# Kernel tuning notes

Measured on AMD Instinct MI355X. Metric: run time of the kernel, lower is better.

Reference implementation:

```python
import jax, jax.numpy as jnp
import numpy as np


def setup_inputs() -> dict:
    key = jax.random.key(0)
    x = jax.random.normal(key, (4, 5, 256, 32, 32), dtype=jnp.float32)
    return {"x": x, "beta": 1}


def reference(x, beta):
    # x: [B, L, D, H, W] -> [B, L, H, W, D] -> [B, L, N, D], N = H*W
    B, L, D, H, W = x.shape
    xf = jnp.transpose(x, (0, 1, 3, 4, 2)).reshape(B, L, H * W, D)
    # scores: [B, L, N, N]
    scores = jnp.einsum('blnd,blmd->blnm', xf, xf)
    # exp(beta*s)/sum == softmax(beta*s) along last axis (numerically stable form)
    attention = jax.nn.softmax(beta * scores, axis=-1)
    # (x.unsqueeze(2) * attn.unsqueeze(4)).sum(3) == attn @ x
    return jnp.einsum('blnm,blmd->blnd', attention, xf)
```

## Files before the change

kernel.cpp:

```cpp
#include <hip/hip_runtime.h>


typedef __attribute__((ext_vector_type(8))) short bf16x8;
typedef __attribute__((ext_vector_type(4))) float f32x4;
typedef __attribute__((ext_vector_type(16))) float f32x16;

#define GLD16(gp, lp) __builtin_amdgcn_global_load_lds( \
    (const __attribute__((address_space(1))) unsigned int*)(const void*)(gp), \
    (__attribute__((address_space(3))) unsigned int*)(void*)(lp), 16, 0, 0)

#define LDS_BARRIER() __asm__ volatile("s_waitcnt lgkmcnt(0)\ns_barrier" ::: "memory")
#define MEMFENCE()    __asm__ volatile("" ::: "memory")
#define WAIT_KDMA()   do { __asm__ volatile("s_waitcnt vmcnt(8)" ::: "memory"); \
                           __builtin_amdgcn_sched_barrier(0); } while (0)

__device__ __forceinline__ unsigned int pack_bf16_rne(float a, float b) {
    unsigned int ua = __float_as_uint(a); ua += 0x7FFFu + ((ua >> 16) & 1u);
    unsigned int ub = __float_as_uint(b); ub += 0x7FFFu + ((ub >> 16) & 1u);
    return (ua >> 16) | (ub & 0xFFFF0000u);
}
__device__ __forceinline__ unsigned int pack2_trunc(float lo, float hi) {
    return __builtin_amdgcn_perm(__float_as_uint(hi), __float_as_uint(lo), 0x07060302u);
}

__global__ __launch_bounds__(256) void prep_kernel(const float* __restrict__ x,
                                                   unsigned short* __restrict__ XT,
                                                   unsigned short* __restrict__ XV) {
    __shared__ __align__(16) unsigned char smem[16384];
    int bid = blockIdx.x;
    int t = threadIdx.x;
    if (bid < 640) {
        uint4* T = (uint4*)smem;
        int slice = bid >> 5, w = bid & 31;
        int cc0 = (w & 3) * 32, d0 = (w >> 2) * 32;
        const float* xs = x + slice * 262144;
        int ccl = t & 31, dr = t >> 5;
        #pragma unroll
        for (int p = 0; p < 4; ++p) {
            int dl = p * 8 + dr;
            const float* src = xs + (d0 + dl) * 1024 + (cc0 + ccl) * 8;
            float4 a = *(const float4*)(src);
            float4 b = *(const float4*)(src + 4);
            uint4 o;
            o.x = pack_bf16_rne(a.x, a.y); o.y = pack_bf16_rne(a.z, a.w);
            o.z = pack_bf16_rne(b.x, b.y); o.w = pack_bf16_rne(b.z, b.w);
            T[ccl * 32 + (dl ^ ccl)] = o;
        }
        __syncthreads();
        unsigned short* xv = XV + slice * 262144;
        int dl2 = t & 31, cr = t >> 5;
        #pragma unroll
        for (int p = 0; p < 4; ++p) {
            int ccl2 = p * 8 + cr;
            uint4 o = T[ccl2 * 32 + (dl2 ^ ccl2)];
            *(uint4*)(xv + ((cc0 + ccl2) * 256 + d0 + dl2) * 8) = o;
        }
    } else {
        unsigned long long* TX = (unsigned long long*)smem;
        int b = bid - 640;
        int slice = b >> 5, w = b & 31;
        int d0 = (w & 1) * 128, n0 = (w >> 1) * 64;
        const float* xs = x + slice * 262144;
        int nq = t & 15, dqh = t >> 4;
        #pragma unroll
        for (int p = 0; p < 2; ++p) {
            int dq = p * 16 + dqh;
            const float* src = xs + (d0 + dq * 4) * 1024 + n0 + nq * 4;
            float4 r0 = *(const float4*)(src);
            float4 r1 = *(const float4*)(src + 1024);
            float4 r2 = *(const float4*)(src + 2048);
            float4 r3 = *(const float4*)(src + 3072);
            const float* f0 = (const float*)&r0; const float* f1 = (const float*)&r1;
            const float* f2 = (const float*)&r2; const float* f3 = (const float*)&r3;
            #pragma unroll
            for (int j = 0; j < 4; ++j) {
                int nl2 = nq * 4 + j;
                unsigned long long q = (unsigned long long)pack_bf16_rne(f0[j], f1[j])
                    | ((unsigned long long)pack_bf16_rne(f2[j], f3[j]) << 32);
                TX[nl2 * 32 + (dq ^ (nl2 & 31))] = q;
            }
        }
        __syncthreads();
        unsigned short* xt = XT + slice * 262144;
        int ch = t & 15, nr = t >> 4;
        #pragma unroll
        for (int p = 0; p < 4; ++p) {
            int nl2 = p * 16 + nr;
            unsigned long long qlo = TX[nl2 * 32 + ((ch * 2) ^ (nl2 & 31))];
            unsigned long long qhi = TX[nl2 * 32 + ((ch * 2 + 1) ^ (nl2 & 31))];
            uint4 o = make_uint4((unsigned int)qlo, (unsigned int)(qlo >> 32),
                                 (unsigned int)qhi, (unsigned int)(qhi >> 32));
            *(uint4*)(xt + (n0 + nl2) * 256 + ((((d0 >> 3) + ch) ^ (nl2 & 7)) * 8)) = o;
        }
    }
}

__global__ __launch_bounds__(256, 2) void attn_kernel(const unsigned short* __restrict__ XT,
                                                      const unsigned short* __restrict__ XV,
                                                      const int* __restrict__ beta,
                                                      float* __restrict__ out) {
    __shared__ __align__(16) unsigned short Kmd[64 * 256];
    __shared__ __align__(16) unsigned short Qlds[48 * 256];
    __shared__ __align__(16) unsigned short Pb[2][64 * 64];
    float* Lpart = (float*)&Pb[0][0];
    float* Ltot  = (float*)&Pb[0][2048];

    int bid = blockIdx.x;
    int t = ((bid & 7) * 40) + (bid >> 3);
    int slice = t >> 4, qh = t & 15;

    int tid = threadIdx.x;
    int lane = tid & 63, wv = tid >> 6;
    int nl = lane & 15, g = lane >> 4;
    int lo = lane & 31, hi = lane >> 5;

    const unsigned short* xt_s = XT + slice * 262144;
    const unsigned short* xv_s = XV + slice * 262144;
    float cscale = (float)(beta[0]) * 1.44269504089f;

    auto kdma = [&](int kt) {
        const unsigned short* gk = xt_s + kt * 16384;
        #pragma unroll
        for (int i = 0; i < 8; ++i) {
            int ch = wv * 8 + i;
            GLD16(gk + ch * 512 + lane * 8, &Kmd[ch * 512]);
        }
    };

    kdma(0);
    {
        const unsigned short* gq = xt_s + (qh * 64 + 16) * 256;
        #pragma unroll
        for (int i = 0; i < 6; ++i) {
            int ch = wv * 6 + i;
            GLD16(gq + ch * 512 + lane * 8, &Qlds[ch * 512]);
        }
    }
    MEMFENCE();

    bf16x8 qf[8];
    float mcol[4];
    {
        int n = qh * 64 + nl;
        const unsigned short* qrow = xt_s + n * 256;
        float dg = 0.f;
        #pragma unroll
        for (int ks = 0; ks < 8; ++ks) {
            qf[ks] = *(const bf16x8*)(qrow + (((ks * 4 + g) ^ (n & 7)) * 8));
            const unsigned int* qu = (const unsigned int*)&qf[ks];
            #pragma unroll
            for (int w = 0; w < 4; ++w) {
                float flo = __uint_as_float(qu[w] << 16);
                float fhi = __uint_as_float(qu[w] & 0xFFFF0000u);
                dg = fmaf(flo, flo, dg);
                dg = fmaf(fhi, fhi, dg);
            }
        }
        dg += __shfl_xor(dg, 16);
        dg += __shfl_xor(dg, 32);
        mcol[0] = dg * cscale;
    }

    const unsigned short* vb = xv_s + (hi * 256 + wv * 64 + lo) * 8;
    bf16x8 vf[8];
    MEMFENCE();
    #pragma unroll
    for (int ks = 0; ks < 4; ++ks) {
        vf[ks * 2]     = *(const bf16x8*)(vb + ks * 4096);
        vf[ks * 2 + 1] = *(const bf16x8*)(vb + ks * 4096 + 256);
    }
    __asm__ volatile("s_waitcnt vmcnt(8)" ::: "memory");
    __builtin_amdgcn_sched_barrier(0);
    LDS_BARRIER();

    #pragma unroll
    for (int st = 1; st < 4; ++st) {
        const unsigned short* qrow = &Qlds[((st - 1) * 16 + nl) * 256];
        float dg = 0.f;
        #pragma unroll
        for (int ks = 0; ks < 8; ++ks) {
            bf16x8 qv = *(const bf16x8*)(qrow + (((ks * 4 + g) ^ (nl & 7)) * 8));
            const unsigned int* qu = (const unsigned int*)&qv;
            #pragma unroll
            for (int w = 0; w < 4; ++w) {
                float flo = __uint_as_float(qu[w] << 16);
                float fhi = __uint_as_float(qu[w] & 0xFFFF0000u);
                dg = fmaf(flo, flo, dg);
                dg = fmaf(fhi, fhi, dg);
            }
        }
        dg += __shfl_xor(dg, 16);
        dg += __shfl_xor(dg, 32);
        mcol[st] = dg * cscale;
    }

    f32x16 acc[2][2];
    acc[0][0] = (f32x16)(0.f); acc[0][1] = (f32x16)(0.f);
    acc[1][0] = (f32x16)(0.f); acc[1][1] = (f32x16)(0.f);
    float lac[4] = {0.f, 0.f, 0.f, 0.f};

    const unsigned short* kmd_row = &Kmd[(wv * 16 + nl) * 256];
    const unsigned short* q1 = &Qlds[nl * 256];
    const unsigned short* q2 = &Qlds[(16 + nl) * 256];
    const unsigned short* q3 = &Qlds[(32 + nl) * 256];

    for (int kt = 0; kt < 16; ++kt) {
        WAIT_KDMA();

        f32x4 s0 = {0.f,0.f,0.f,0.f}, s1 = {0.f,0.f,0.f,0.f};
        f32x4 s2 = {0.f,0.f,0.f,0.f}, s3 = {0.f,0.f,0.f,0.f};
        #pragma unroll
        for (int ks = 0; ks < 8; ++ks) {
            int ch = ((ks * 4 + g) ^ (nl & 7)) * 8;
            bf16x8 af = *(const bf16x8*)(kmd_row + ch);
            s0 = __builtin_amdgcn_mfma_f32_16x16x32_bf16(af, qf[ks], s0, 0, 0, 0);
            s1 = __builtin_amdgcn_mfma_f32_16x16x32_bf16(af, *(const bf16x8*)(q1 + ch), s1, 0, 0, 0);
            s2 = __builtin_amdgcn_mfma_f32_16x16x32_bf16(af, *(const bf16x8*)(q2 + ch), s2, 0, 0, 0);
            s3 = __builtin_amdgcn_mfma_f32_16x16x32_bf16(af, *(const bf16x8*)(q3 + ch), s3, 0, 0, 0);
        }

        {
            f32x4 sv[4] = {s0, s1, s2, s3};
            #pragma unroll
            for (int st = 0; st < 4; ++st) {
                float p0 = exp2f(fmaf(sv[st][0], cscale, -mcol[st]));
                float p1 = exp2f(fmaf(sv[st][1], cscale, -mcol[st]));
                float p2 = exp2f(fmaf(sv[st][2], cscale, -mcol[st]));
                float p3 = exp2f(fmaf(sv[st][3], cscale, -mcol[st]));
                lac[st] += (p0 + p1) + (p2 + p3);
                *(uint2*)(&Pb[kt & 1][(st * 16 + nl) * 64 +
                                      (((wv * 2 + (g >> 1)) ^ (nl & 7)) * 8) + (g & 1) * 4]) =
                    make_uint2(pack2_trunc(p0, p1), pack2_trunc(p2, p3));
            }
        }

        if (kt < 15) kdma(kt + 1);
        MEMFENCE();

        LDS_BARRIER();

        {
            const unsigned short* vnext = vb + (kt + 1) * 16384;
            #pragma unroll
            for (int ks = 0; ks < 4; ++ks) {
                int ch = ((ks * 2 + hi) ^ (lo & 7)) * 8;
                bf16x8 pf0 = *(const bf16x8*)(&Pb[kt & 1][lo * 64 + ch]);
                bf16x8 pf1 = *(const bf16x8*)(&Pb[kt & 1][(32 + lo) * 64 + ch]);
                acc[0][0] = __builtin_amdgcn_mfma_f32_32x32x16_bf16(pf0, vf[ks * 2],     acc[0][0], 0, 0, 0);
                acc[0][1] = __builtin_amdgcn_mfma_f32_32x32x16_bf16(pf0, vf[ks * 2 + 1], acc[0][1], 0, 0, 0);
                acc[1][0] = __builtin_amdgcn_mfma_f32_32x32x16_bf16(pf1, vf[ks * 2],     acc[1][0], 0, 0, 0);
                acc[1][1] = __builtin_amdgcn_mfma_f32_32x32x16_bf16(pf1, vf[ks * 2 + 1], acc[1][1], 0, 0, 0);
                if (kt < 15) {
                    vf[ks * 2]     = *(const bf16x8*)(vnext + ks * 4096);
                    vf[ks * 2 + 1] = *(const bf16x8*)(vnext + ks * 4096 + 256);
                }
            }
        }
    }

    #pragma unroll
    for (int st = 0; st < 4; ++st) {
        lac[st] += __shfl_xor(lac[st], 16);
        lac[st] += __shfl_xor(lac[st], 32);
    }
    if (lane < 16) {
        #pragma unroll
        for (int st = 0; st < 4; ++st) Lpart[wv * 64 + st * 16 + nl] = lac[st];
    }
    LDS_BARRIER();
    if (tid < 64)
        Ltot[tid] = 1.f / (Lpart[tid] + Lpart[64 + tid] + Lpart[128 + tid] + Lpart[192 + tid]);
    LDS_BARRIER();

    float* outs = out + slice * 262144 + (qh * 64) * 256;
    #pragma unroll
    for (int nb = 0; nb < 2; ++nb) {
        #pragma unroll
        for (int rq = 0; rq < 4; ++rq) {
            f32x4 li = *(const f32x4*)(&Ltot[nb * 32 + rq * 8 + hi * 4]);
            #pragma unroll
            for (int j = 0; j < 4; ++j) {
                int row = nb * 32 + rq * 8 + hi * 4 + j;
                #pragma unroll
                for (int dt = 0; dt < 2; ++dt)
                    outs[row * 256 + wv * 64 + dt * 32 + lo] = acc[nb][dt][rq * 4 + j] * li[j];
            }
        }
    }
}

extern "C" void kernel_launch(void* const* d_in, const int* in_sizes, int n_in,
                              void* d_out, int out_size, void* d_ws, size_t ws_size,
                              hipStream_t stream) {
    const float* x = (const float*)d_in[0];
    const int* beta = (const int*)d_in[1];
    float* out = (float*)d_out;
    unsigned short* XT = (unsigned short*)d_ws;
    unsigned short* XV = (unsigned short*)d_ws + 5242880;
    prep_kernel<<<1280, 256, 0, stream>>>(x, XT, XV);
    attn_kernel<<<320, 256, 0, stream>>>(XT, XV, beta, out);
}
```

Measured before the change: 118.2 us.

## Keep all Q fragments in registers and split V prefetch to drop Qlds

Loads all four 16-row Q tiles directly from global into registers instead of staging three of them in LDS. This removes the 24KB Qlds buffer and the per-iteration LDS reads of Q in the score MFMA loop. V fragments are now split: half is prefetched across iterations and the other half is loaded in the current iteration, which lowers register pressure to make room for the larger Q set. The vmcnt wait drops to 4 to match the smaller outstanding-load count. The trade-off is more exposed global-load latency on the in-iteration V half and a higher VGPR count, which could limit occupancy at 2 blocks per CU.

```diff
diff --git a/kernel.cpp b/kernel.cpp
--- a/kernel.cpp
+++ b/kernel.cpp
@@ -11,7 +11,7 @@
 
 #define LDS_BARRIER() __asm__ volatile("s_waitcnt lgkmcnt(0)\ns_barrier" ::: "memory")
 #define MEMFENCE()    __asm__ volatile("" ::: "memory")
-#define WAIT_KDMA()   do { __asm__ volatile("s_waitcnt vmcnt(8)" ::: "memory"); \
+#define WAIT_KDMA()   do { __asm__ volatile("s_waitcnt vmcnt(4)" ::: "memory"); \
                            __builtin_amdgcn_sched_barrier(0); } while (0)
 
 __device__ __forceinline__ unsigned int pack_bf16_rne(float a, float b) {
@@ -100,10 +100,9 @@
                                                       const int* __restrict__ beta,
                                                       float* __restrict__ out) {
     __shared__ __align__(16) unsigned short Kmd[64 * 256];
-    __shared__ __align__(16) unsigned short Qlds[48 * 256];
     __shared__ __align__(16) unsigned short Pb[2][64 * 64];
-    float* Lpart = (float*)&Pb[0][0];
-    float* Ltot  = (float*)&Pb[0][2048];
+    __shared__ float Lpart[4][64];
+    __shared__ __align__(16) float Ltot[64];
 
     int bid = blockIdx.x;
     int t = ((bid & 7) * 40) + (bid >> 3);
@@ -128,26 +127,19 @@
     };
 
     kdma(0);
-    {
-        const unsigned short* gq = xt_s + (qh * 64 + 16) * 256;
-        #pragma unroll
-        for (int i = 0; i < 6; ++i) {
-            int ch = wv * 6 + i;
-            GLD16(gq + ch * 512 + lane * 8, &Qlds[ch * 512]);
-        }
-    }
     MEMFENCE();
 
-    bf16x8 qf[8];
+    bf16x8 qf[4][8];
     float mcol[4];
-    {
-        int n = qh * 64 + nl;
+    #pragma unroll
+    for (int st = 0; st < 4; ++st) {
+        int n = qh * 64 + st * 16 + nl;
         const unsigned short* qrow = xt_s + n * 256;
         float dg = 0.f;
         #pragma unroll
         for (int ks = 0; ks < 8; ++ks) {
-            qf[ks] = *(const bf16x8*)(qrow + (((ks * 4 + g) ^ (n & 7)) * 8));
-            const unsigned int* qu = (const unsigned int*)&qf[ks];
+            qf[st][ks] = *(const bf16x8*)(qrow + (((ks * 4 + g) ^ (n & 7)) * 8));
+            const unsigned int* qu = (const unsigned int*)&qf[st][ks];
             #pragma unroll
             for (int w = 0; w < 4; ++w) {
                 float flo = __uint_as_float(qu[w] << 16);
@@ -158,39 +150,6 @@
         }
         dg += __shfl_xor(dg, 16);
         dg += __shfl_xor(dg, 32);
-        mcol[0] = dg * cscale;
-    }
-
-    const unsigned short* vb = xv_s + (hi * 256 + wv * 64 + lo) * 8;
-    bf16x8 vf[8];
-    MEMFENCE();
-    #pragma unroll
-    for (int ks = 0; ks < 4; ++ks) {
-        vf[ks * 2]     = *(const bf16x8*)(vb + ks * 4096);
-        vf[ks * 2 + 1] = *(const bf16x8*)(vb + ks * 4096 + 256);
-    }
-    __asm__ volatile("s_waitcnt vmcnt(8)" ::: "memory");
-    __builtin_amdgcn_sched_barrier(0);
-    LDS_BARRIER();
-
-    #pragma unroll
-    for (int st = 1; st < 4; ++st) {
-        const unsigned short* qrow = &Qlds[((st - 1) * 16 + nl) * 256];
-        float dg = 0.f;
-        #pragma unroll
-        for (int ks = 0; ks < 8; ++ks) {
-            bf16x8 qv = *(const bf16x8*)(qrow + (((ks * 4 + g) ^ (nl & 7)) * 8));
-            const unsigned int* qu = (const unsigned int*)&qv;
-            #pragma unroll
-            for (int w = 0; w < 4; ++w) {
-                float flo = __uint_as_float(qu[w] << 16);
-                float fhi = __uint_as_float(qu[w] & 0xFFFF0000u);
-                dg = fmaf(flo, flo, dg);
-                dg = fmaf(fhi, fhi, dg);
-            }
-        }
-        dg += __shfl_xor(dg, 16);
-        dg += __shfl_xor(dg, 32);
         mcol[st] = dg * cscale;
     }
 
@@ -199,10 +158,13 @@
     acc[1][0] = (f32x16)(0.f); acc[1][1] = (f32x16)(0.f);
     float lac[4] = {0.f, 0.f, 0.f, 0.f};
 
+    const unsigned short* vb = xv_s + (hi * 256 + wv * 64 + lo) * 8;
+    bf16x8 vf0[4];
+    MEMFENCE();
+    #pragma unroll
+    for (int ks = 0; ks < 4; ++ks) vf0[ks] = *(const bf16x8*)(vb + ks * 4096);
+
     const unsigned short* kmd_row = &Kmd[(wv * 16 + nl) * 256];
-    const unsigned short* q1 = &Qlds[nl * 256];
-    const unsigned short* q2 = &Qlds[(16 + nl) * 256];
-    const unsigned short* q3 = &Qlds[(32 + nl) * 256];
 
     for (int kt = 0; kt < 16; ++kt) {
         WAIT_KDMA();
@@ -211,12 +173,11 @@
         f32x4 s2 = {0.f,0.f,0.f,0.f}, s3 = {0.f,0.f,0.f,0.f};
         #pragma unroll
         for (int ks = 0; ks < 8; ++ks) {
-            int ch = ((ks * 4 + g) ^ (nl & 7)) * 8;
-            bf16x8 af = *(const bf16x8*)(kmd_row + ch);
-            s0 = __builtin_amdgcn_mfma_f32_16x16x32_bf16(af, qf[ks], s0, 0, 0, 0);
-            s1 = __builtin_amdgcn_mfma_f32_16x16x32_bf16(af, *(const bf16x8*)(q1 + ch), s1, 0, 0, 0);
-            s2 = __builtin_amdgcn_mfma_f32_16x16x32_bf16(af, *(const bf16x8*)(q2 + ch), s2, 0, 0, 0);
-            s3 = __builtin_amdgcn_mfma_f32_16x16x32_bf16(af, *(const bf16x8*)(q3 + ch), s3, 0, 0, 0);
+            bf16x8 af = *(const bf16x8*)(kmd_row + (((ks * 4 + g) ^ (nl & 7)) * 8));
+            s0 = __builtin_amdgcn_mfma_f32_16x16x32_bf16(af, qf[0][ks], s0, 0, 0, 0);
+            s1 = __builtin_amdgcn_mfma_f32_16x16x32_bf16(af, qf[1][ks], s1, 0, 0, 0);
+            s2 = __builtin_amdgcn_mfma_f32_16x16x32_bf16(af, qf[2][ks], s2, 0, 0, 0);
+            s3 = __builtin_amdgcn_mfma_f32_16x16x32_bf16(af, qf[3][ks], s3, 0, 0, 0);
         }
 
         {
@@ -240,20 +201,30 @@
         LDS_BARRIER();
 
         {
-            const unsigned short* vnext = vb + (kt + 1) * 16384;
+            const unsigned short* vcur = vb + kt * 16384;
+            const unsigned short* vnxt = vb + (kt + 1) * 16384;
+            bf16x8 vf1[4];
+            #pragma unroll
+            for (int ks = 0; ks < 4; ++ks) vf1[ks] = *(const bf16x8*)(vcur + ks * 4096 + 256);
             #pragma unroll
             for (int ks = 0; ks < 4; ++ks) {
                 int ch = ((ks * 2 + hi) ^ (lo & 7)) * 8;
                 bf16x8 pf0 = *(const bf16x8*)(&Pb[kt & 1][lo * 64 + ch]);
                 bf16x8 pf1 = *(const bf16x8*)(&Pb[kt & 1][(32 + lo) * 64 + ch]);
-                acc[0][0] = __builtin_amdgcn_mfma_f32_32x32x16_bf16(pf0, vf[ks * 2],     acc[0][0], 0, 0, 0);
-                acc[0][1] = __builtin_amdgcn_mfma_f32_32x32x16_bf16(pf0, vf[ks * 2 + 1], acc[0][1], 0, 0, 0);
-                acc[1][0] = __builtin_amdgcn_mfma_f32_32x32x16_bf16(pf1, vf[ks * 2],     acc[1][0], 0, 0, 0);
-                acc[1][1] = __builtin_amdgcn_mfma_f32_32x32x16_bf16(pf1, vf[ks * 2 + 1], acc[1][1], 0, 0, 0);
-                if (kt < 15) {
-                    vf[ks * 2]     = *(const bf16x8*)(vnext + ks * 4096);
-                    vf[ks * 2 + 1] = *(const bf16x8*)(vnext + ks * 4096 + 256);
-                }
+                acc[0][0] = __builtin_amdgcn_mfma_f32_32x32x16_bf16(pf0, vf0[ks], acc[0][0], 0, 0, 0);
+                acc[1][0] = __builtin_amdgcn_mfma_f32_32x32x16_bf16(pf1, vf0[ks], acc[1][0], 0, 0, 0);
+            }
+            if (kt < 15) {
+                #pragma unroll
+                for (int ks = 0; ks < 4; ++ks) vf0[ks] = *(const bf16x8*)(vnxt + ks * 4096);
+            }
+            #pragma unroll
+            for (int ks = 0; ks < 4; ++ks) {
+                int ch = ((ks * 2 + hi) ^ (lo & 7)) * 8;
+                bf16x8 pf0 = *(const bf16x8*)(&Pb[kt & 1][lo * 64 + ch]);
+                bf16x8 pf1 = *(const bf16x8*)(&Pb[kt & 1][(32 + lo) * 64 + ch]);
+                acc[0][1] = __builtin_amdgcn_mfma_f32_32x32x16_bf16(pf0, vf1[ks], acc[0][1], 0, 0, 0);
+                acc[1][1] = __builtin_amdgcn_mfma_f32_32x32x16_bf16(pf1, vf1[ks], acc[1][1], 0, 0, 0);
             }
         }
     }
@@ -265,11 +236,11 @@
     }
     if (lane < 16) {
         #pragma unroll
-        for (int st = 0; st < 4; ++st) Lpart[wv * 64 + st * 16 + nl] = lac[st];
+        for (int st = 0; st < 4; ++st) Lpart[wv][st * 16 + nl] = lac[st];
     }
     LDS_BARRIER();
     if (tid < 64)
-        Ltot[tid] = 1.f / (Lpart[tid] + Lpart[64 + tid] + Lpart[128 + tid] + Lpart[192 + tid]);
+        Ltot[tid] = 1.f / (Lpart[0][tid] + Lpart[1][tid] + Lpart[2][tid] + Lpart[3][tid]);
     LDS_BARRIER();
 
     float* outs = out + slice * 262144 + (qh * 64) * 256;
@@ -282,8 +253,8 @@
             for (int j = 0; j < 4; ++j) {
                 int row = nb * 32 + rq * 8 + hi * 4 + j;
                 #pragma unroll
-                for (int dt = 0; dt < 2; ++dt)
-                    outs[row * 256 + wv * 64 + dt * 32 + lo] = acc[nb][dt][rq * 4 + j] * li[j];
+                for (int db = 0; db < 2; ++db)
+                    outs[row * 256 + wv * 64 + db * 32 + lo] = acc[nb][db][rq * 4 + j] * li[j];
             }
         }
     }
```

Result: slower. 141.0 us (+19.3%).
